# Optimization experiments

Hardware: AMD Instinct MI355X
Metric: run time of the kernel (lower is better)

Reference implementation:

```python
import jax, jax.numpy as jnp
import numpy as np

B, C, H, W = 32, 3072, 28, 28
L1 = 9            # num_landmarks + 1 (background)
NUM_CLASSES = 200


def setup_inputs() -> dict:
    key = jax.random.key(0)
    k1, k2, k3 = jax.random.split(key, 3)
    feat = jax.random.normal(k1, (B, C, H, W), dtype=jnp.float32)
    w_land = jax.random.normal(k2, (L1, C), dtype=jnp.float32) * 0.02  # fc_landmarks 1x1 conv weight
    modulation = jnp.ones((1, C, L1), dtype=jnp.float32)
    w_cls = jax.random.normal(k3, (NUM_CLASSES, C), dtype=jnp.float32) * 0.02
    return {"feat": feat, "w_land": w_land, "modulation": modulation, "w_cls": w_cls}


def reference(feat, w_land, modulation, w_cls):
    # fc_landmarks: 1x1 conv == per-pixel GEMM. ab: (B, L1, H, W)
    ab = jnp.einsum('bchw,lc->blhw', feat, w_land)
    # squared distance to each landmark 'code': ||x||^2 - 2<x,w> + ||w||^2
    b_sq = jnp.sum(feat * feat, axis=1, keepdims=True)            # (B,1,H,W)
    a_sq = jnp.sum(w_land * w_land, axis=1)[None, :, None, None]  # (1,L1,1,1)
    dist = b_sq - 2.0 * ab + a_sq                                 # (B,L1,H,W)
    maps = jax.nn.softmax(-dist, axis=1)                          # softmax over landmarks
    # (maps.unsqueeze(1) * x.unsqueeze(2)).mean(-1).mean(-1)  ->  weighted spatial pooling
    # expressed as a contraction instead of materializing (B,C,L1,H,W)
    all_features = jnp.einsum('bchw,blhw->bcl', feat, maps) / (H * W)  # (B,C,L1)
    all_features_mod = all_features * modulation                       # 'original' modulation
    # drop background landmark, linear classifier per landmark (eval: dropout = identity)
    scores = jnp.einsum('bcl,kc->bkl', all_features_mod[..., :-1], w_cls)  # (B,num_classes,L)
    # modulation_orth = False -> return all_features (pre-modulation)
    return (all_features, maps, scores, dist)
```

## Files before the change

### kernel.cpp

```cpp
#include <hip/hip_runtime.h>

#define BB 32
#define CC 3072
#define HWD 784
#define L1 9
#define NCLS 200
#define CSPLIT 32
#define CCHUNK 96
#define WROW 12

#define AF_OFF     0
#define MAPS_OFF   884736
#define SCORES_OFF 1110528
#define DIST_OFF   1161728

#define P_OFF   0
#define P_CNT   (BB*CSPLIT*10*HWD)
#define WT_OFF  (P_OFF + P_CNT)
#define WT_CNT  (CC*WROW)
#define ASQ_OFF (WT_OFF + WT_CNT)
#define ASQ_CNT (12*WROW)
#define AFT_OFF (ASQ_OFF + ASQ_CNT)

__global__ __launch_bounds__(256) void kW(const float* __restrict__ w_land,
                                          float* __restrict__ wT,
                                          float* __restrict__ asqp) {
    __shared__ float red[4][L1];
    const int tid = threadIdx.x;
    const int c = blockIdx.x * 256 + tid;
    float w[L1], s[L1];
    #pragma unroll
    for (int l = 0; l < L1; ++l) w[l] = w_land[l * CC + c];
    #pragma unroll
    for (int l = 0; l < L1; ++l) { wT[c * WROW + l] = w[l]; s[l] = w[l] * w[l]; }
    wT[c * WROW + 9] = 0.f; wT[c * WROW + 10] = 0.f; wT[c * WROW + 11] = 0.f;
    #pragma unroll
    for (int l = 0; l < L1; ++l) {
        float v = s[l];
        for (int off = 32; off; off >>= 1) v += __shfl_xor(v, off);
        s[l] = v;
    }
    const int lane = tid & 63, wv = tid >> 6;
    if (lane == 0) {
        #pragma unroll
        for (int l = 0; l < L1; ++l) red[wv][l] = s[l];
    }
    __syncthreads();
    if (tid == 0) {
        #pragma unroll
        for (int l = 0; l < L1; ++l)
            asqp[blockIdx.x * WROW + l] = red[0][l] + red[1][l] + red[2][l] + red[3][l];
    }
}

__global__ __launch_bounds__(256) void kA(const float* __restrict__ feat,
                                          const float* __restrict__ wT,
                                          float* __restrict__ partial) {
    const int tid = threadIdx.x;
    if (tid >= HWD / 4) return;
    const int b = blockIdx.x, cs = blockIdx.y;
    const int p4 = tid * 4;
    const float* fp = feat + ((size_t)b * CC + (size_t)cs * CCHUNK) * HWD + p4;
    const float* wp = wT + (size_t)cs * CCHUNK * WROW;

    float abx[L1], aby[L1], abz[L1], abw[L1];
    #pragma unroll
    for (int l = 0; l < L1; ++l) { abx[l] = 0.f; aby[l] = 0.f; abz[l] = 0.f; abw[l] = 0.f; }
    float bx = 0.f, by = 0.f, bz = 0.f, bw = 0.f;

    #pragma unroll 4
    for (int c = 0; c < CCHUNK; ++c) {
        const float4 f = *(const float4*)&fp[(size_t)c * HWD];
        bx += f.x * f.x; by += f.y * f.y; bz += f.z * f.z; bw += f.w * f.w;
        #pragma unroll
        for (int l = 0; l < L1; ++l) {
            const float w = wp[c * WROW + l];
            abx[l] += f.x * w; aby[l] += f.y * w; abz[l] += f.z * w; abw[l] += f.w * w;
        }
    }
    float* pout = partial + (size_t)(b * CSPLIT + cs) * 10 * HWD + p4;
    #pragma unroll
    for (int l = 0; l < L1; ++l) {
        float4 o; o.x = abx[l]; o.y = aby[l]; o.z = abz[l]; o.w = abw[l];
        *(float4*)&pout[(size_t)l * HWD] = o;
    }
    float4 o; o.x = bx; o.y = by; o.z = bz; o.w = bw;
    *(float4*)&pout[(size_t)9 * HWD] = o;
}

__global__ __launch_bounds__(256) void kB(const float* __restrict__ partial,
                                          const float* __restrict__ asqp,
                                          float* __restrict__ maps_out,
                                          float* __restrict__ dist_out) {
    const int b = blockIdx.x >> 2, pb = blockIdx.x & 3;
    const int pix = pb * 256 + threadIdx.x;
    if (pix >= HWD) return;

    float asq[L1];
    #pragma unroll
    for (int l = 0; l < L1; ++l) {
        float s = 0.f;
        #pragma unroll
        for (int bc = 0; bc < 12; ++bc) s += asqp[bc * WROW + l];
        asq[l] = s;
    }

    float ab[L1], bsq = 0.f;
    #pragma unroll
    for (int l = 0; l < L1; ++l) ab[l] = 0.f;
    const float* pp = partial + (size_t)b * CSPLIT * 10 * HWD + pix;
    #pragma unroll 4
    for (int cs = 0; cs < CSPLIT; ++cs) {
        const float* q = pp + (size_t)cs * 10 * HWD;
        #pragma unroll
        for (int l = 0; l < L1; ++l) ab[l] += q[(size_t)l * HWD];
        bsq += q[(size_t)9 * HWD];
    }

    float d[L1], mn = 1e30f;
    #pragma unroll
    for (int l = 0; l < L1; ++l) {
        d[l] = bsq - 2.f * ab[l] + asq[l];
        mn = fminf(mn, d[l]);
    }
    float e[L1], sum = 0.f;
    #pragma unroll
    for (int l = 0; l < L1; ++l) {
        e[l] = __expf(mn - d[l]);
        sum += e[l];
    }
    const float inv = 1.f / sum;
    #pragma unroll
    for (int l = 0; l < L1; ++l) {
        const size_t o = ((size_t)b * L1 + l) * HWD + pix;
        maps_out[o] = e[l] * inv;
        dist_out[o] = d[l];
    }
}

__global__ __launch_bounds__(256) void kC(const float* __restrict__ feat,
                                          const float* __restrict__ maps,
                                          const float* __restrict__ modulation,
                                          float* __restrict__ af_out,
                                          float* __restrict__ afT) {
    const int wv = threadIdx.x >> 6, lane = threadIdx.x & 63;
    const int b = blockIdx.y;
    const int c0 = blockIdx.x * 16 + wv * 4;
    const float* fb = feat + ((size_t)b * CC + c0) * HWD;
    const float* mb = maps + (size_t)b * L1 * HWD;

    float acc[4][L1];
    #pragma unroll
    for (int j = 0; j < 4; ++j)
        #pragma unroll
        for (int l = 0; l < L1; ++l) acc[j][l] = 0.f;

    for (int g = lane; g < HWD / 4; g += 64) {
        const int p4 = g * 4;
        float4 m4[L1];
        #pragma unroll
        for (int l = 0; l < L1; ++l) m4[l] = *(const float4*)&mb[(size_t)l * HWD + p4];
        #pragma unroll
        for (int j = 0; j < 4; ++j) {
            const float4 f = *(const float4*)&fb[(size_t)j * HWD + p4];
            #pragma unroll
            for (int l = 0; l < L1; ++l)
                acc[j][l] += f.x * m4[l].x + f.y * m4[l].y + f.z * m4[l].z + f.w * m4[l].w;
        }
    }
    #pragma unroll
    for (int j = 0; j < 4; ++j)
        #pragma unroll
        for (int l = 0; l < L1; ++l) {
            float v = acc[j][l];
            for (int off = 32; off; off >>= 1) v += __shfl_xor(v, off);
            acc[j][l] = v;
        }
    if (lane == 0) {
        #pragma unroll
        for (int j = 0; j < 4; ++j) {
            const int c = c0 + j;
            #pragma unroll
            for (int l = 0; l < L1; ++l) {
                const float v = acc[j][l] * (1.f / (float)HWD);
                af_out[((size_t)b * CC + c) * L1 + l] = v;
                if (l < 8)
                    afT[((size_t)b * 8 + l) * CC + c] = v * modulation[c * L1 + l];
            }
        }
    }
}

__global__ __launch_bounds__(256) void kD(const float* __restrict__ afT,
                                          const float* __restrict__ w_cls,
                                          float* __restrict__ scores) {
    const int wid = blockIdx.x * 4 + (threadIdx.x >> 6);
    const int lane = threadIdx.x & 63;
    const int b = wid / (NCLS / 2), kp = wid - b * (NCLS / 2);
    const int k0 = kp * 2;
    const float* at = afT + (size_t)b * 8 * CC;
    const float* w0 = w_cls + (size_t)k0 * CC;
    const float* w1 = w0 + CC;

    float acc[2][8];
    #pragma unroll
    for (int kk = 0; kk < 2; ++kk)
        #pragma unroll
        for (int l = 0; l < 8; ++l) acc[kk][l] = 0.f;

    #pragma unroll 2
    for (int it = 0; it < CC / 256; ++it) {
        const int c4 = (lane + it * 64) * 4;
        const float4 wa = *(const float4*)&w0[c4];
        const float4 wb = *(const float4*)&w1[c4];
        #pragma unroll
        for (int l = 0; l < 8; ++l) {
            const float4 a = *(const float4*)&at[(size_t)l * CC + c4];
            acc[0][l] += wa.x * a.x + wa.y * a.y + wa.z * a.z + wa.w * a.w;
            acc[1][l] += wb.x * a.x + wb.y * a.y + wb.z * a.z + wb.w * a.w;
        }
    }
    #pragma unroll
    for (int kk = 0; kk < 2; ++kk)
        #pragma unroll
        for (int l = 0; l < 8; ++l) {
            float v = acc[kk][l];
            for (int off = 32; off; off >>= 1) v += __shfl_xor(v, off);
            acc[kk][l] = v;
        }
    if (lane == 0) {
        #pragma unroll
        for (int kk = 0; kk < 2; ++kk)
            #pragma unroll
            for (int l = 0; l < 8; ++l)
                scores[((size_t)b * NCLS + k0 + kk) * 8 + l] = acc[kk][l];
    }
}

extern "C" void kernel_launch(void* const* d_in, const int* in_sizes, int n_in,
                              void* d_out, int out_size, void* d_ws, size_t ws_size,
                              hipStream_t stream) {
    const float* feat       = (const float*)d_in[0];
    const float* w_land     = (const float*)d_in[1];
    const float* modulation = (const float*)d_in[2];
    const float* w_cls      = (const float*)d_in[3];

    float* out    = (float*)d_out;
    float* af     = out + AF_OFF;
    float* maps   = out + MAPS_OFF;
    float* scores = out + SCORES_OFF;
    float* dist   = out + DIST_OFF;

    float* ws      = (float*)d_ws;
    float* partial = ws + P_OFF;
    float* wT      = ws + WT_OFF;
    float* asqp    = ws + ASQ_OFF;
    float* afT     = ws + AFT_OFF;

    kW<<<CC / 256, 256, 0, stream>>>(w_land, wT, asqp);
    kA<<<dim3(BB, CSPLIT), 256, 0, stream>>>(feat, wT, partial);
    kB<<<BB * 4, 256, 0, stream>>>(partial, asqp, maps, dist);
    kC<<<dim3(CC / 16, BB), 256, 0, stream>>>(feat, maps, modulation, af, afT);
    kD<<<BB * NCLS / 2 / 4, 256, 0, stream>>>(afT, w_cls, scores);
}
```

Measured before the change: 519.5 us.

## Stage feature tiles in LDS for pooling kernel and halve kA channel split

The pooling kernel kC now handles 128 channels per block. It stages 112-pixel feature tiles into padded shared memory, and each thread accumulates two channel rows across a quarter of the pixel range. A final LDS reduction then combines the four waves. This replaces per-wave shuffle reductions and repeated loads of the maps array for every 4 channels, giving more reuse of the maps loads. Separately, kA's channel split drops from 32 to 16 with larger chunks, which means fewer partial sums to reduce but less parallelism. The maps reads are now scalar per-pixel loads with broadcast-style access, and the smaller grid (24x32 blocks) may limit occupancy.

```diff
diff --git a/kernel.cpp b/kernel.cpp
--- a/kernel.cpp
+++ b/kernel.cpp
@@ -5,8 +5,8 @@
 #define HWD 784
 #define L1 9
 #define NCLS 200
-#define CSPLIT 32
-#define CCHUNK 96
+#define CSPLIT 16
+#define CCHUNK 192
 #define WROW 12
 
 #define AF_OFF     0
@@ -138,56 +138,68 @@
     }
 }
 
+#define KCH 128
+#define KCK 112
+#define KST 113
 __global__ __launch_bounds__(256) void kC(const float* __restrict__ feat,
                                           const float* __restrict__ maps,
                                           const float* __restrict__ modulation,
                                           float* __restrict__ af_out,
                                           float* __restrict__ afT) {
-    const int wv = threadIdx.x >> 6, lane = threadIdx.x & 63;
+    __shared__ float fs[KCH * KST];
+    const int tid = threadIdx.x;
     const int b = blockIdx.y;
-    const int c0 = blockIdx.x * 16 + wv * 4;
+    const int c0 = blockIdx.x * KCH;
+    const int w = __builtin_amdgcn_readfirstlane(tid >> 6);
+    const int lane = tid & 63;
     const float* fb = feat + ((size_t)b * CC + c0) * HWD;
-    const float* mb = maps + (size_t)b * L1 * HWD;
-
-    float acc[4][L1];
-    #pragma unroll
-    for (int j = 0; j < 4; ++j)
-        #pragma unroll
-        for (int l = 0; l < L1; ++l) acc[j][l] = 0.f;
-
-    for (int g = lane; g < HWD / 4; g += 64) {
-        const int p4 = g * 4;
-        float4 m4[L1];
-        #pragma unroll
-        for (int l = 0; l < L1; ++l) m4[l] = *(const float4*)&mb[(size_t)l * HWD + p4];
-        #pragma unroll
-        for (int j = 0; j < 4; ++j) {
-            const float4 f = *(const float4*)&fb[(size_t)j * HWD + p4];
+    const float* mbase = maps + (size_t)b * L1 * HWD;
+
+    float acc0[L1], acc1[L1];
+    #pragma unroll
+    for (int l = 0; l < L1; ++l) { acc0[l] = 0.f; acc1[l] = 0.f; }
+
+    for (int k = 0; k < HWD / KCK; ++k) {
+        for (int i = tid; i < KCH * KCK / 2; i += 256) {
+            const int row = i / (KCK / 2);
+            const int p2 = i - row * (KCK / 2);
+            const float2 v = *(const float2*)&fb[(size_t)row * HWD + k * KCK + p2 * 2];
+            fs[row * KST + p2 * 2]     = v.x;
+            fs[row * KST + p2 * 2 + 1] = v.y;
+        }
+        __syncthreads();
+        const float* mp = mbase + k * KCK + w * (KCK / 4);
+        const float* r0 = &fs[lane * KST + w * (KCK / 4)];
+        const float* r1 = &fs[(lane + 64) * KST + w * (KCK / 4)];
+        #pragma unroll 4
+        for (int p = 0; p < KCK / 4; ++p) {
+            float m[L1];
             #pragma unroll
-            for (int l = 0; l < L1; ++l)
-                acc[j][l] += f.x * m4[l].x + f.y * m4[l].y + f.z * m4[l].z + f.w * m4[l].w;
-        }
-    }
-    #pragma unroll
-    for (int j = 0; j < 4; ++j)
-        #pragma unroll
-        for (int l = 0; l < L1; ++l) {
-            float v = acc[j][l];
-            for (int off = 32; off; off >>= 1) v += __shfl_xor(v, off);
-            acc[j][l] = v;
-        }
-    if (lane == 0) {
-        #pragma unroll
-        for (int j = 0; j < 4; ++j) {
-            const int c = c0 + j;
+            for (int l = 0; l < L1; ++l) m[l] = mp[(size_t)l * HWD + p];
+            const float f0 = r0[p], f1 = r1[p];
             #pragma unroll
-            for (int l = 0; l < L1; ++l) {
-                const float v = acc[j][l] * (1.f / (float)HWD);
-                af_out[((size_t)b * CC + c) * L1 + l] = v;
-                if (l < 8)
-                    afT[((size_t)b * 8 + l) * CC + c] = v * modulation[c * L1 + l];
-            }
-        }
+            for (int l = 0; l < L1; ++l) { acc0[l] += f0 * m[l]; acc1[l] += f1 * m[l]; }
+        }
+        __syncthreads();
+    }
+
+    #pragma unroll
+    for (int l = 0; l < L1; ++l) {
+        fs[w * 1152 + l * 64 + lane]       = acc0[l];
+        fs[w * 1152 + 576 + l * 64 + lane] = acc1[l];
+    }
+    __syncthreads();
+    for (int idx = tid; idx < 1152; idx += 256) {
+        const int j = idx / 576;
+        const int rem = idx - j * 576;
+        const int l = rem >> 6;
+        const int cl = rem & 63;
+        const int c = c0 + j * 64 + cl;
+        const float s = (fs[idx] + fs[1152 + idx] + fs[2304 + idx] + fs[3456 + idx])
+                        * (1.f / (float)HWD);
+        af_out[((size_t)b * CC + c) * L1 + l] = s;
+        if (l < 8)
+            afT[((size_t)b * 8 + l) * CC + c] = s * modulation[c * L1 + l];
     }
 }
 
@@ -260,6 +272,6 @@
     kW<<<CC / 256, 256, 0, stream>>>(w_land, wT, asqp);
     kA<<<dim3(BB, CSPLIT), 256, 0, stream>>>(feat, wT, partial);
     kB<<<BB * 4, 256, 0, stream>>>(partial, asqp, maps, dist);
-    kC<<<dim3(CC / 16, BB), 256, 0, stream>>>(feat, maps, modulation, af, afT);
+    kC<<<dim3(CC / KCH, BB), 256, 0, stream>>>(feat, maps, modulation, af, afT);
     kD<<<BB * NCLS / 2 / 4, 256, 0, stream>>>(afT, w_cls, scores);
 }
```

Result: slower. 660.7 us (+27.2%).
